# Kernel optimization log

Measured on AMD Instinct MI355X. Metric: run time of the kernel, lower is better.

The kernel has to match this reference:

```python
import jax, jax.numpy as jnp
import numpy as np

B, T, C = 2, 2048, 768
N_HEADS = 12
D_K = C // N_HEADS  # 64


def setup_inputs() -> dict:
    key = jax.random.key(0)
    k1, k2, k3, k4, k5 = jax.random.split(key, 5)
    x = jax.random.normal(k1, (B, T, C), dtype=jnp.float32)
    # glorot-normal-ish scaled params
    query_mat = jax.random.normal(k2, (C, N_HEADS, D_K), dtype=jnp.float32) * (2.0 / (C + D_K)) ** 0.5
    key_mat = jax.random.normal(k3, (C, N_HEADS, D_K), dtype=jnp.float32) * (2.0 / (C + D_K)) ** 0.5
    value_mat = jax.random.normal(k4, (C, N_HEADS, D_K), dtype=jnp.float32) * (2.0 / (C + D_K)) ** 0.5
    linear_m1 = jax.random.normal(k5, (C, C), dtype=jnp.float32) * (2.0 / (C + C)) ** 0.5
    return {"x": x, "query_mat": query_mat, "key_mat": key_mat,
            "value_mat": value_mat, "linear_m1": linear_m1}


def reference(x, query_mat, key_mat, value_mat, linear_m1):
    b, t, c = x.shape
    h, d_k = query_mat.shape[1], query_mat.shape[2]
    q = jnp.einsum('btc,chd->bhtd', x, query_mat)
    k = jnp.einsum('btc,chd->bhtd', x, key_mat)
    v = jnp.einsum('btc,chd->bhtd', x, value_mat)
    # NOTE: original module MULTIPLIES by sqrt(d_k) (not divides) - kept faithful.
    w = jnp.einsum('bhtd,bhzd->bhtz', q, k) * (d_k ** 0.5)
    causal = jnp.tril(jnp.ones((t, t), dtype=bool))  # [T,T], True on/below diag
    w = jnp.where(causal, w, -jnp.inf)
    w = jax.nn.softmax(w, axis=-1)
    o = jnp.einsum('bhtz,bhzd->bhtd', w, v)
    o = jnp.transpose(o, (0, 2, 1, 3)).reshape(b, t, h * d_k)
    return jnp.einsum('btc,cz->btz', o, linear_m1)
```

## Files before the change

kernel.cpp:

```cpp
#include <hip/hip_runtime.h>
#include <hip/hip_bf16.h>


typedef float f32x4 __attribute__((ext_vector_type(4)));
typedef short s16x8 __attribute__((ext_vector_type(8)));

#define MFMA(a, b, c) __builtin_amdgcn_mfma_f32_16x16x32_bf16((a), (b), (c), 0, 0, 0)

constexpr int Bb = 2, Tt = 2048, Cc = 768, Hh = 12, Dd = 64;
constexpr int Mm = Bb * Tt;
constexpr int BH = Bb * Hh;

__device__ __forceinline__ void gload16(const void* g, void* l) {
  __builtin_amdgcn_global_load_lds((const __attribute__((address_space(1))) void*)g,
                                   (__attribute__((address_space(3))) void*)l, 16, 0, 0);
}

__device__ __forceinline__ short f2bfbits(float f) {
  __hip_bfloat16 h = __float2bfloat16(f);
  return __builtin_bit_cast(short, h);
}
__device__ __forceinline__ float bf2f(short s) {
  __hip_bfloat16 h = __builtin_bit_cast(__hip_bfloat16, s);
  return __bfloat162float(h);
}
__device__ __forceinline__ unsigned int packbf2(float a, float b) {
  return (unsigned int)(unsigned short)f2bfbits(a) |
         ((unsigned int)(unsigned short)f2bfbits(b) << 16);
}

__global__ __launch_bounds__(256) void prep_x(const float* __restrict__ x,
                                              __hip_bfloat16* __restrict__ xhi,
                                              __hip_bfloat16* __restrict__ xlo) {
  const size_t i = ((size_t)blockIdx.x * 256 + threadIdx.x) * 8;
  float4 a = *reinterpret_cast<const float4*>(x + i);
  float4 b = *reinterpret_cast<const float4*>(x + i + 4);
  float v[8] = {a.x, a.y, a.z, a.w, b.x, b.y, b.z, b.w};
  s16x8 hi, lo;
#pragma unroll
  for (int j = 0; j < 8; ++j) {
    short h = f2bfbits(v[j]);
    hi[j] = h;
    lo[j] = f2bfbits(v[j] - bf2f(h));
  }
  *reinterpret_cast<s16x8*>((short*)xhi + i) = hi;
  *reinterpret_cast<s16x8*>((short*)xlo + i) = lo;
}

__global__ __launch_bounds__(256) void prep_w(
    const float* __restrict__ s0, const float* __restrict__ s1,
    const float* __restrict__ s2, const float* __restrict__ s3,
    __hip_bfloat16* __restrict__ h0, __hip_bfloat16* __restrict__ l0,
    __hip_bfloat16* __restrict__ h1, __hip_bfloat16* __restrict__ l1,
    __hip_bfloat16* __restrict__ h2, __hip_bfloat16* __restrict__ h3) {
  const float* src;
  __hip_bfloat16 *dh, *dl = nullptr;
  switch (blockIdx.z) {
    case 0: src = s0; dh = h0; dl = l0; break;
    case 1: src = s1; dh = h1; dl = l1; break;
    case 2: src = s2; dh = h2; break;
    default: src = s3; dh = h3; break;
  }
  __shared__ float tile[64][65];
  const int r0 = blockIdx.y * 64, c0 = blockIdx.x * 64;
  const int tid = threadIdx.x;
  const int rr = tid >> 4, c4 = (tid & 15) * 4;
#pragma unroll
  for (int it = 0; it < 4; ++it) {
    float4 v = *reinterpret_cast<const float4*>(src + (size_t)(r0 + rr + it * 16) * Cc + c0 + c4);
    tile[rr + it * 16][c4 + 0] = v.x;
    tile[rr + it * 16][c4 + 1] = v.y;
    tile[rr + it * 16][c4 + 2] = v.z;
    tile[rr + it * 16][c4 + 3] = v.w;
  }
  __syncthreads();
#pragma unroll
  for (int it = 0; it < 2; ++it) {
    const int id = tid + it * 256;
    const int n = id >> 3, ch = (id & 7) * 8;
    s16x8 hi, lo;
#pragma unroll
    for (int j = 0; j < 8; ++j) {
      float v = tile[ch + j][n];
      short h = f2bfbits(v);
      hi[j] = h;
      lo[j] = f2bfbits(v - bf2f(h));
    }
    *reinterpret_cast<s16x8*>(dh + (size_t)(c0 + n) * Cc + r0 + ch) = hi;
    if (dl) *reinterpret_cast<s16x8*>(dl + (size_t)(c0 + n) * Cc + r0 + ch) = lo;
  }
}

__device__ __forceinline__ void gemm128_core(const __hip_bfloat16* __restrict__ A,
                                             const __hip_bfloat16* __restrict__ Bt,
                                             int m0, int n0,
                                             short* ldsA, short* ldsB,
                                             f32x4 acc[4][4]) {
  const int tid = threadIdx.x;
  const int w = tid >> 6, l = tid & 63;
  const int wr = w >> 1, wc = w & 1;
  const int srow = l >> 2;
  const int scol = (l & 3) << 3;

  for (int kt = 0; kt < Cc / 32; ++kt) {
    const int kk = kt << 5;
#pragma unroll
    for (int i = 0; i < 2; ++i) {
      const int r = (w << 5) + (i << 4);
      gload16(A + (size_t)(m0 + r + srow) * Cc + kk + scol, ldsA + r * 32);
      gload16(Bt + (size_t)(n0 + r + srow) * Cc + kk + scol, ldsB + r * 32);
    }
    __syncthreads();
    s16x8 af[4], bfr[4];
#pragma unroll
    for (int i = 0; i < 4; ++i) {
      af[i]  = *reinterpret_cast<const s16x8*>(ldsA + ((wr << 6) + (i << 4) + (l & 15)) * 32 + ((l >> 4) << 3));
      bfr[i] = *reinterpret_cast<const s16x8*>(ldsB + ((wc << 6) + (i << 4) + (l & 15)) * 32 + ((l >> 4) << 3));
    }
#pragma unroll
    for (int i = 0; i < 4; ++i)
#pragma unroll
      for (int j = 0; j < 4; ++j)
        acc[i][j] = MFMA(af[i], bfr[j], acc[i][j]);
    __syncthreads();
  }
}

__device__ __forceinline__ void gemm128_hilo(
    const __hip_bfloat16* __restrict__ Ahi, const __hip_bfloat16* __restrict__ Alo,
    const __hip_bfloat16* __restrict__ Bhi, const __hip_bfloat16* __restrict__ Blo,
    bool lo, int m0, int n0, short* lds, f32x4 acc[4][4]) {
  short* ldsAh = lds;
  short* ldsAl = lds + 4096;
  short* ldsBh = lds + 8192;
  short* ldsBl = lds + 12288;
  const int tid = threadIdx.x;
  const int w = tid >> 6, l = tid & 63;
  const int wr = w >> 1, wc = w & 1;
  const int srow = l >> 2;
  const int scol = (l & 3) << 3;

  for (int kt = 0; kt < Cc / 32; ++kt) {
    const int kk = kt << 5;
#pragma unroll
    for (int i = 0; i < 2; ++i) {
      const int r = (w << 5) + (i << 4);
      const size_t aoff = (size_t)(m0 + r + srow) * Cc + kk + scol;
      const size_t boff = (size_t)(n0 + r + srow) * Cc + kk + scol;
      gload16(Ahi + aoff, ldsAh + r * 32);
      gload16(Bhi + boff, ldsBh + r * 32);
      if (lo) {
        gload16(Alo + aoff, ldsAl + r * 32);
        gload16(Blo + boff, ldsBl + r * 32);
      }
    }
    __syncthreads();
    s16x8 ah[4], bh[4], al[4], bl[4];
#pragma unroll
    for (int i = 0; i < 4; ++i) {
      const int ao = ((wr << 6) + (i << 4) + (l & 15)) * 32 + ((l >> 4) << 3);
      const int bo = ((wc << 6) + (i << 4) + (l & 15)) * 32 + ((l >> 4) << 3);
      ah[i] = *reinterpret_cast<const s16x8*>(ldsAh + ao);
      bh[i] = *reinterpret_cast<const s16x8*>(ldsBh + bo);
      if (lo) {
        al[i] = *reinterpret_cast<const s16x8*>(ldsAl + ao);
        bl[i] = *reinterpret_cast<const s16x8*>(ldsBl + bo);
      }
    }
#pragma unroll
    for (int i = 0; i < 4; ++i)
#pragma unroll
      for (int j = 0; j < 4; ++j)
        acc[i][j] = MFMA(ah[i], bh[j], acc[i][j]);
    if (lo) {
#pragma unroll
      for (int i = 0; i < 4; ++i)
#pragma unroll
        for (int j = 0; j < 4; ++j) {
          acc[i][j] = MFMA(ah[i], bl[j], acc[i][j]);
          acc[i][j] = MFMA(al[i], bh[j], acc[i][j]);
        }
    }
    __syncthreads();
  }
}

__global__ __launch_bounds__(256) void qkv_gemm(
    const __hip_bfloat16* __restrict__ Xhi, const __hip_bfloat16* __restrict__ Xlo,
    const __hip_bfloat16* __restrict__ WqThi, const __hip_bfloat16* __restrict__ WqTlo,
    const __hip_bfloat16* __restrict__ WkThi, const __hip_bfloat16* __restrict__ WkTlo,
    const __hip_bfloat16* __restrict__ WvThi,
    __hip_bfloat16* __restrict__ Qhi, __hip_bfloat16* __restrict__ Qlo,
    __hip_bfloat16* __restrict__ Khi, __hip_bfloat16* __restrict__ Klo,
    __hip_bfloat16* __restrict__ V) {
  __shared__ __align__(16) short lds[16384];
  const int z = blockIdx.z;
  const bool lo = (z < 2);
  const __hip_bfloat16* Bhi = (z == 0) ? WqThi : (z == 1) ? WkThi : WvThi;
  const __hip_bfloat16* Blo = (z == 0) ? WqTlo : WkTlo;
  const int m0 = blockIdx.x * 128, n0 = blockIdx.y * 128;

  f32x4 acc[4][4];
#pragma unroll
  for (int i = 0; i < 4; ++i)
#pragma unroll
    for (int j = 0; j < 4; ++j) acc[i][j] = f32x4{0.f, 0.f, 0.f, 0.f};

  gemm128_hilo(Xhi, Xlo, Bhi, Blo, lo, m0, n0, lds, acc);

  const int tid = threadIdx.x, w = tid >> 6, l = tid & 63;
  const int wr = w >> 1, wc = w & 1;
#pragma unroll
  for (int i = 0; i < 4; ++i) {
#pragma unroll
    for (int j = 0; j < 4; ++j) {
#pragma unroll
      for (int r = 0; r < 4; ++r) {
        const int m = m0 + (wr << 6) + (i << 4) + ((l >> 4) << 2) + r;
        const int n = n0 + (wc << 6) + (j << 4) + (l & 15);
        const float v = acc[i][j][r];
        const int b = m >> 11, t = m & 2047, h = n >> 6, d = n & 63;
        const size_t idx = (((size_t)(b * Hh + h)) * Tt + t) * Dd + d;
        if (z == 2) {
          V[idx] = __float2bfloat16(v);
        } else {
          short hbits = f2bfbits(v);
          short lbits = f2bfbits(v - bf2f(hbits));
          if (z == 0) { ((short*)Qhi)[idx] = hbits; ((short*)Qlo)[idx] = lbits; }
          else        { ((short*)Khi)[idx] = hbits; ((short*)Klo)[idx] = lbits; }
        }
      }
    }
  }
}

__global__ __launch_bounds__(256) void proj_gemm(
    const __hip_bfloat16* __restrict__ O, const __hip_bfloat16* __restrict__ LT,
    float* __restrict__ out) {
  __shared__ __align__(16) short lds[8192];
  const int m0 = blockIdx.x * 128, n0 = blockIdx.y * 128;
  f32x4 acc[4][4];
#pragma unroll
  for (int i = 0; i < 4; ++i)
#pragma unroll
    for (int j = 0; j < 4; ++j) acc[i][j] = f32x4{0.f, 0.f, 0.f, 0.f};

  gemm128_core(O, LT, m0, n0, lds, lds + 4096, acc);

  const int tid = threadIdx.x, w = tid >> 6, l = tid & 63;
  const int wr = w >> 1, wc = w & 1;
#pragma unroll
  for (int i = 0; i < 4; ++i)
#pragma unroll
    for (int j = 0; j < 4; ++j)
#pragma unroll
      for (int r = 0; r < 4; ++r) {
        const int m = m0 + (wr << 6) + (i << 4) + ((l >> 4) << 2) + r;
        const int n = n0 + (wc << 6) + (j << 4) + (l & 15);
        out[(size_t)m * Cc + n] = acc[i][j][r];
      }
}

__global__ __launch_bounds__(256) void transpose_v(
    const __hip_bfloat16* __restrict__ V, __hip_bfloat16* __restrict__ VT) {
  __shared__ __align__(16) short tile[64][72];
  const int t0 = blockIdx.x * 64, bh = blockIdx.y;
  const __hip_bfloat16* src = V + (size_t)bh * Tt * Dd;
  __hip_bfloat16* dst = VT + (size_t)bh * Dd * Tt;
  const int tid = threadIdx.x;
  const int rr = tid >> 3;
  const int cc = (tid & 7) << 3;
#pragma unroll
  for (int it = 0; it < 2; ++it) {
    const int r = rr + it * 32;
    *reinterpret_cast<s16x8*>(&tile[r][cc]) =
        *reinterpret_cast<const s16x8*>(src + (size_t)(t0 + r) * Dd + cc);
  }
  __syncthreads();
#pragma unroll
  for (int it = 0; it < 2; ++it) {
    const int d = rr + it * 32;
    s16x8 o;
#pragma unroll
    for (int j = 0; j < 8; ++j) o[j] = tile[cc + j][d];
    *reinterpret_cast<s16x8*>(dst + (size_t)d * Tt + t0 + cc) = o;
  }
}

__global__ __launch_bounds__(256, 2) void attn_fwd(
    const __hip_bfloat16* __restrict__ Qhi, const __hip_bfloat16* __restrict__ Qlo,
    const __hip_bfloat16* __restrict__ Khi, const __hip_bfloat16* __restrict__ Klo,
    const __hip_bfloat16* __restrict__ VT, __hip_bfloat16* __restrict__ O) {
  __shared__ __align__(16) short kv[2][3][4096];
  __shared__ __align__(16) short pbuf[4][16 * 72];
  const int i = blockIdx.x;
  const int j = i >> 3;
  const int bh = (i & 7) * 3 + (j >> 5);
  const int qblk = 31 - (j & 31);
  const int b = bh / Hh, h = bh % Hh;
  const int tid = threadIdx.x, w = tid >> 6, l = tid & 63;
  const int lr = l & 15, lg = l >> 4;
  const int q0 = qblk * 64 + w * 16;
  const size_t hqk = (size_t)bh * Tt * Dd;
  const __hip_bfloat16* qhp = Qhi + hqk;
  const __hip_bfloat16* qlp = Qlo + hqk;
  const __hip_bfloat16* khp = Khi + hqk;
  const __hip_bfloat16* klp = Klo + hqk;
  const __hip_bfloat16* vtp = VT + (size_t)bh * Dd * Tt;
  short* myP = &pbuf[w][0];
  short* obase = (short*)O + (size_t)b * Tt * Cc + h * Dd;

  const int rr = l >> 3;
  const int gg = (l & 7) ^ rr;

  auto stage = [&](int buf, int k0) {
#pragma unroll
    for (int s6 = 0; s6 < 6; ++s6) {
      const int s = w * 6 + s6;
      const int m = s >> 3, i2 = s & 7;
      const int row = i2 * 8 + rr;
      const __hip_bfloat16* src =
          (m == 0) ? khp + (size_t)(k0 + row) * Dd + gg * 8
        : (m == 1) ? klp + (size_t)(k0 + row) * Dd + gg * 8
                   : vtp + (size_t)row * Tt + k0 + gg * 8;
      gload16(src, &kv[buf][m][i2 * 512]);
    }
  };

  stage(0, 0);

  s16x8 qh[2], ql[2];
#pragma unroll
  for (int df = 0; df < 2; ++df) {
    const size_t off = (size_t)(q0 + lr) * Dd + df * 32 + lg * 8;
    qh[df] = *reinterpret_cast<const s16x8*>(qhp + off);
    ql[df] = *reinterpret_cast<const s16x8*>(qlp + off);
  }

  f32x4 oacc[4];
#pragma unroll
  for (int df = 0; df < 4; ++df) oacc[df] = f32x4{0.f, 0.f, 0.f, 0.f};
  float mrow = -__builtin_inff(), lrow = 0.f;

  __syncthreads();

  const int sw = lr & 7;
  for (int kt = 0; kt <= qblk; ++kt) {
    const int cur = kt & 1;
    const int k0 = kt << 6;
    if (kt < qblk) stage(cur ^ 1, (kt + 1) << 6);

    const short* Kh = &kv[cur][0][0];
    const short* Kl = &kv[cur][1][0];
    const short* Vv = &kv[cur][2][0];
    const bool dotmask = (k0 + 63) > q0;

    f32x4 s[4];
#pragma unroll
    for (int kjf = 0; kjf < 4; ++kjf) s[kjf] = f32x4{0.f, 0.f, 0.f, 0.f};
#pragma unroll
    for (int kjf = 0; kjf < 4; ++kjf)
#pragma unroll
      for (int df = 0; df < 2; ++df) {
        const int off = (kjf * 16 + lr) * 64 + (((df * 4 + lg) ^ sw) << 3);
        const s16x8 kh = *reinterpret_cast<const s16x8*>(Kh + off);
        const s16x8 kl = *reinterpret_cast<const s16x8*>(Kl + off);
        s[kjf] = MFMA(kh, qh[df], s[kjf]);
        s[kjf] = MFMA(kl, qh[df], s[kjf]);
        s[kjf] = MFMA(kh, ql[df], s[kjf]);
      }

    const int q = q0 + lr;
    float mx = -__builtin_inff();
#pragma unroll
    for (int kjf = 0; kjf < 4; ++kjf)
#pragma unroll
      for (int r = 0; r < 4; ++r) {
        float v = s[kjf][r] * 8.0f;
        if (dotmask && (k0 + kjf * 16 + lg * 4 + r) > q) v = -__builtin_inff();
        s[kjf][r] = v;
        mx = fmaxf(mx, v);
      }
    mx = fmaxf(mx, __shfl_xor(mx, 16));
    mx = fmaxf(mx, __shfl_xor(mx, 32));
    const float mnew = fmaxf(mrow, mx);
    const float sc = __expf(mrow - mnew);
    mrow = mnew;
    float ls = 0.f;
#pragma unroll
    for (int kjf = 0; kjf < 4; ++kjf)
#pragma unroll
      for (int r = 0; r < 4; ++r) {
        const float p = __expf(s[kjf][r] - mnew);
        s[kjf][r] = p;
        ls += p;
      }
    ls += __shfl_xor(ls, 16);
    ls += __shfl_xor(ls, 32);
    lrow = lrow * sc + ls;
#pragma unroll
    for (int df = 0; df < 4; ++df) oacc[df] *= sc;

#pragma unroll
    for (int kjf = 0; kjf < 4; ++kjf) {
      uint2 pk;
      pk.x = packbf2(s[kjf][0], s[kjf][1]);
      pk.y = packbf2(s[kjf][2], s[kjf][3]);
      *reinterpret_cast<uint2*>(myP + lr * 72 + kjf * 16 + lg * 4) = pk;
    }

#pragma unroll
    for (int kf = 0; kf < 2; ++kf) {
      const s16x8 pa = *reinterpret_cast<const s16x8*>(myP + lr * 72 + kf * 32 + lg * 8);
#pragma unroll
      for (int df = 0; df < 4; ++df) {
        const int off = (df * 16 + lr) * 64 + (((kf * 4 + lg) ^ sw) << 3);
        const s16x8 bv = *reinterpret_cast<const s16x8*>(Vv + off);
        oacc[df] = MFMA(bv, pa, oacc[df]);
      }
    }

    __syncthreads();
  }

  const float inv = 1.0f / lrow;
  const int t = q0 + lr;
#pragma unroll
  for (int df = 0; df < 4; ++df) {
    uint2 pk;
    pk.x = packbf2(oacc[df][0] * inv, oacc[df][1] * inv);
    pk.y = packbf2(oacc[df][2] * inv, oacc[df][3] * inv);
    *reinterpret_cast<uint2*>(obase + (size_t)t * Cc + df * 16 + lg * 4) = pk;
  }
}

extern "C" void kernel_launch(void* const* d_in, const int* in_sizes, int n_in,
                              void* d_out, int out_size, void* d_ws, size_t ws_size,
                              hipStream_t stream) {
  (void)in_sizes; (void)n_in; (void)out_size; (void)ws_size;
  const float* x  = (const float*)d_in[0];
  const float* wq = (const float*)d_in[1];
  const float* wk = (const float*)d_in[2];
  const float* wv = (const float*)d_in[3];
  const float* lm = (const float*)d_in[4];
  float* out = (float*)d_out;
  __hip_bfloat16* ws = (__hip_bfloat16*)d_ws;

  const size_t WSZ = (size_t)Cc * Cc;
  const size_t TSZ = (size_t)Mm * Cc;
  __hip_bfloat16* WqThi = ws;
  __hip_bfloat16* WqTlo = WqThi + WSZ;
  __hip_bfloat16* WkThi = WqTlo + WSZ;
  __hip_bfloat16* WkTlo = WkThi + WSZ;
  __hip_bfloat16* WvThi = WkTlo + WSZ;
  __hip_bfloat16* LThi  = WvThi + WSZ;
  __hip_bfloat16* Xhi   = LThi + WSZ;
  __hip_bfloat16* Xlo   = Xhi + TSZ;
  __hip_bfloat16* Qhi   = Xlo + TSZ;
  __hip_bfloat16* Qlo   = Qhi + TSZ;
  __hip_bfloat16* Khi   = Qlo + TSZ;
  __hip_bfloat16* Klo   = Khi + TSZ;
  __hip_bfloat16* Vb    = Klo + TSZ;
  __hip_bfloat16* VT    = Vb + TSZ;
  __hip_bfloat16* Ob    = Vb;

  prep_x<<<dim3(Mm * Cc / (256 * 8)), 256, 0, stream>>>(x, Xhi, Xlo);
  prep_w<<<dim3(12, 12, 4), 256, 0, stream>>>(wq, wk, wv, lm,
                                              WqThi, WqTlo, WkThi, WkTlo, WvThi, LThi);
  qkv_gemm<<<dim3(32, 6, 3), 256, 0, stream>>>(Xhi, Xlo, WqThi, WqTlo, WkThi, WkTlo,
                                               WvThi, Qhi, Qlo, Khi, Klo, Vb);
  transpose_v<<<dim3(32, BH), 256, 0, stream>>>(Vb, VT);
  attn_fwd<<<dim3(768), 256, 0, stream>>>(Qhi, Qlo, Khi, Klo, VT, Ob);
  proj_gemm<<<dim3(32, 6), 256, 0, stream>>>(Ob, LThi, out);
}
```

Measured before the change: 139.8 us.

## Single-buffer V in attention, fold scale into Q, merge prep kernels, rebalance tiles

The two prep kernels become one launch. The sqrt(d_k) scale is folded into Q when the QKV GEMM writes it out, and attention LDS use drops by single-buffering V, with V loaded after K and gated by explicit vmcnt waits. That lets launch bounds rise to 3 blocks per CU, and the query-block order is interleaved heavy/light with a per-head offset to balance causal work. The costs are weaker V prefetch overlap, hand-written waitcnt assumptions, and a slight change in Q rounding from scaling before the hi/lo split.

```diff
diff --git a/kernel.cpp b/kernel.cpp
--- a/kernel.cpp
+++ b/kernel.cpp
@@ -29,40 +29,44 @@
          ((unsigned int)(unsigned short)f2bfbits(b) << 16);
 }
 
-__global__ __launch_bounds__(256) void prep_x(const float* __restrict__ x,
-                                              __hip_bfloat16* __restrict__ xhi,
-                                              __hip_bfloat16* __restrict__ xlo) {
-  const size_t i = ((size_t)blockIdx.x * 256 + threadIdx.x) * 8;
-  float4 a = *reinterpret_cast<const float4*>(x + i);
-  float4 b = *reinterpret_cast<const float4*>(x + i + 4);
-  float v[8] = {a.x, a.y, a.z, a.w, b.x, b.y, b.z, b.w};
-  s16x8 hi, lo;
-#pragma unroll
-  for (int j = 0; j < 8; ++j) {
-    short h = f2bfbits(v[j]);
-    hi[j] = h;
-    lo[j] = f2bfbits(v[j] - bf2f(h));
-  }
-  *reinterpret_cast<s16x8*>((short*)xhi + i) = hi;
-  *reinterpret_cast<s16x8*>((short*)xlo + i) = lo;
-}
-
-__global__ __launch_bounds__(256) void prep_w(
+__global__ __launch_bounds__(256) void prep_all(
+    const float* __restrict__ x,
     const float* __restrict__ s0, const float* __restrict__ s1,
     const float* __restrict__ s2, const float* __restrict__ s3,
+    __hip_bfloat16* __restrict__ xhi, __hip_bfloat16* __restrict__ xlo,
     __hip_bfloat16* __restrict__ h0, __hip_bfloat16* __restrict__ l0,
     __hip_bfloat16* __restrict__ h1, __hip_bfloat16* __restrict__ l1,
     __hip_bfloat16* __restrict__ h2, __hip_bfloat16* __restrict__ h3) {
+  __shared__ float tile[64][65];
+  const int bid = blockIdx.x;
+  if (bid < 1536) {
+    const size_t i = ((size_t)bid * 256 + threadIdx.x) * 8;
+    float4 a = *reinterpret_cast<const float4*>(x + i);
+    float4 b = *reinterpret_cast<const float4*>(x + i + 4);
+    float v[8] = {a.x, a.y, a.z, a.w, b.x, b.y, b.z, b.w};
+    s16x8 hi, lo;
+#pragma unroll
+    for (int j = 0; j < 8; ++j) {
+      short h = f2bfbits(v[j]);
+      hi[j] = h;
+      lo[j] = f2bfbits(v[j] - bf2f(h));
+    }
+    *reinterpret_cast<s16x8*>((short*)xhi + i) = hi;
+    *reinterpret_cast<s16x8*>((short*)xlo + i) = lo;
+    return;
+  }
+  const int q = bid - 1536;
+  const int z = q / 144, rem = q % 144;
+  const int by = rem / 12, bx = rem % 12;
   const float* src;
   __hip_bfloat16 *dh, *dl = nullptr;
-  switch (blockIdx.z) {
+  switch (z) {
     case 0: src = s0; dh = h0; dl = l0; break;
     case 1: src = s1; dh = h1; dl = l1; break;
     case 2: src = s2; dh = h2; break;
     default: src = s3; dh = h3; break;
   }
-  __shared__ float tile[64][65];
-  const int r0 = blockIdx.y * 64, c0 = blockIdx.x * 64;
+  const int r0 = by * 64, c0 = bx * 64;
   const int tid = threadIdx.x;
   const int rr = tid >> 4, c4 = (tid & 15) * 4;
 #pragma unroll
@@ -218,12 +222,13 @@
       for (int r = 0; r < 4; ++r) {
         const int m = m0 + (wr << 6) + (i << 4) + ((l >> 4) << 2) + r;
         const int n = n0 + (wc << 6) + (j << 4) + (l & 15);
-        const float v = acc[i][j][r];
+        float v = acc[i][j][r];
         const int b = m >> 11, t = m & 2047, h = n >> 6, d = n & 63;
         const size_t idx = (((size_t)(b * Hh + h)) * Tt + t) * Dd + d;
         if (z == 2) {
           V[idx] = __float2bfloat16(v);
         } else {
+          if (z == 0) v *= 8.0f;
           short hbits = f2bfbits(v);
           short lbits = f2bfbits(v - bf2f(hbits));
           if (z == 0) { ((short*)Qhi)[idx] = hbits; ((short*)Qlo)[idx] = lbits; }
@@ -287,16 +292,19 @@
   }
 }
 
-__global__ __launch_bounds__(256, 2) void attn_fwd(
+__global__ __launch_bounds__(256, 3) void attn_fwd(
     const __hip_bfloat16* __restrict__ Qhi, const __hip_bfloat16* __restrict__ Qlo,
     const __hip_bfloat16* __restrict__ Khi, const __hip_bfloat16* __restrict__ Klo,
     const __hip_bfloat16* __restrict__ VT, __hip_bfloat16* __restrict__ O) {
-  __shared__ __align__(16) short kv[2][3][4096];
+  __shared__ __align__(16) short kvk[2][2][4096];
+  __shared__ __align__(16) short kvv[4096];
   __shared__ __align__(16) short pbuf[4][16 * 72];
   const int i = blockIdx.x;
   const int j = i >> 3;
-  const int bh = (i & 7) * 3 + (j >> 5);
-  const int qblk = 31 - (j & 31);
+  const int m3 = j >> 5;
+  const int bh = (i & 7) * 3 + m3;
+  const int sp = ((j & 31) + 11 * m3) & 31;
+  const int qblk = (sp & 1) ? (sp >> 1) : (31 - (sp >> 1));
   const int b = bh / Hh, h = bh % Hh;
   const int tid = threadIdx.x, w = tid >> 6, l = tid & 63;
   const int lr = l & 15, lg = l >> 4;
@@ -313,21 +321,29 @@
   const int rr = l >> 3;
   const int gg = (l & 7) ^ rr;
 
-  auto stage = [&](int buf, int k0) {
-#pragma unroll
-    for (int s6 = 0; s6 < 6; ++s6) {
-      const int s = w * 6 + s6;
+  auto stageK = [&](int buf, int k0) {
+#pragma unroll
+    for (int s6 = 0; s6 < 4; ++s6) {
+      const int s = w * 4 + s6;
       const int m = s >> 3, i2 = s & 7;
       const int row = i2 * 8 + rr;
-      const __hip_bfloat16* src =
-          (m == 0) ? khp + (size_t)(k0 + row) * Dd + gg * 8
-        : (m == 1) ? klp + (size_t)(k0 + row) * Dd + gg * 8
-                   : vtp + (size_t)row * Tt + k0 + gg * 8;
-      gload16(src, &kv[buf][m][i2 * 512]);
+      const __hip_bfloat16* src = (m == 0)
+          ? khp + (size_t)(k0 + row) * Dd + gg * 8
+          : klp + (size_t)(k0 + row) * Dd + gg * 8;
+      gload16(src, &kvk[buf][m][i2 * 512]);
     }
   };
-
-  stage(0, 0);
+  auto stageV = [&](int k0) {
+#pragma unroll
+    for (int s6 = 0; s6 < 2; ++s6) {
+      const int i2 = w * 2 + s6;
+      const int row = i2 * 8 + rr;
+      gload16(vtp + (size_t)row * Tt + k0 + gg * 8, &kvv[i2 * 512]);
+    }
+  };
+
+  stageK(0, 0);
+  stageV(0);
 
   s16x8 qh[2], ql[2];
 #pragma unroll
@@ -345,15 +361,15 @@
   __syncthreads();
 
   const int sw = lr & 7;
-  for (int kt = 0; kt <= qblk; ++kt) {
+  const int nt = qblk;
+  for (int kt = 0; kt <= nt; ++kt) {
     const int cur = kt & 1;
     const int k0 = kt << 6;
-    if (kt < qblk) stage(cur ^ 1, (kt + 1) << 6);
-
-    const short* Kh = &kv[cur][0][0];
-    const short* Kl = &kv[cur][1][0];
-    const short* Vv = &kv[cur][2][0];
-    const bool dotmask = (k0 + 63) > q0;
+    if (kt > 0) stageV(k0);
+    if (kt < nt) stageK(cur ^ 1, (kt + 1) << 6);
+
+    const short* Kh = &kvk[cur][0][0];
+    const short* Kl = &kvk[cur][1][0];
 
     f32x4 s[4];
 #pragma unroll
@@ -371,12 +387,13 @@
       }
 
     const int q = q0 + lr;
+    const bool dotmask = (k0 + 63) > q0;
     float mx = -__builtin_inff();
 #pragma unroll
     for (int kjf = 0; kjf < 4; ++kjf)
 #pragma unroll
       for (int r = 0; r < 4; ++r) {
-        float v = s[kjf][r] * 8.0f;
+        float v = s[kjf][r];
         if (dotmask && (k0 + kjf * 16 + lg * 4 + r) > q) v = -__builtin_inff();
         s[kjf][r] = v;
         mx = fmaxf(mx, v);
@@ -409,13 +426,20 @@
       *reinterpret_cast<uint2*>(myP + lr * 72 + kjf * 16 + lg * 4) = pk;
     }
 
+    if (kt < nt) {
+      asm volatile("s_waitcnt vmcnt(4)" ::: "memory");
+    } else {
+      asm volatile("s_waitcnt vmcnt(0)" ::: "memory");
+    }
+    __builtin_amdgcn_sched_barrier(0);
+
 #pragma unroll
     for (int kf = 0; kf < 2; ++kf) {
       const s16x8 pa = *reinterpret_cast<const s16x8*>(myP + lr * 72 + kf * 32 + lg * 8);
 #pragma unroll
       for (int df = 0; df < 4; ++df) {
         const int off = (df * 16 + lr) * 64 + (((kf * 4 + lg) ^ sw) << 3);
-        const s16x8 bv = *reinterpret_cast<const s16x8*>(Vv + off);
+        const s16x8 bv = *reinterpret_cast<const s16x8*>(kvv + off);
         oacc[df] = MFMA(bv, pa, oacc[df]);
       }
     }
@@ -464,9 +488,8 @@
   __hip_bfloat16* VT    = Vb + TSZ;
   __hip_bfloat16* Ob    = Vb;
 
-  prep_x<<<dim3(Mm * Cc / (256 * 8)), 256, 0, stream>>>(x, Xhi, Xlo);
-  prep_w<<<dim3(12, 12, 4), 256, 0, stream>>>(wq, wk, wv, lm,
-                                              WqThi, WqTlo, WkThi, WkTlo, WvThi, LThi);
+  prep_all<<<dim3(2112), 256, 0, stream>>>(x, wq, wk, wv, lm, Xhi, Xlo,
+                                           WqThi, WqTlo, WkThi, WkTlo, WvThi, LThi);
   qkv_gemm<<<dim3(32, 6, 3), 256, 0, stream>>>(Xhi, Xlo, WqThi, WqTlo, WkThi, WkTlo,
                                                WvThi, Qhi, Qlo, Khi, Klo, Vb);
   transpose_v<<<dim3(32, BH), 256, 0, stream>>>(Vb, VT);
```

Result: faster. 133.5 us (-4.5%).
